# Kernel optimization log

Measured on AMD Instinct MI355X. Metric: run time of the kernel, lower is better.

The kernel has to match this reference:

```python
import jax, jax.numpy as jnp
import numpy as np

B, D3, L, H, O, E, GH = 4096, 288, 32, 512, 96, 8, 128


def _init_linear(key, out_dim, in_dim):
    kw, kb = jax.random.split(key)
    bound = 1.0 / np.sqrt(in_dim)
    W = jax.random.uniform(kw, (out_dim, in_dim), jnp.float32, -bound, bound)
    b = jax.random.uniform(kb, (out_dim,), jnp.float32, -bound, bound)
    return W, b


def setup_inputs() -> dict:
    key = jax.random.key(0)
    ks = jax.random.split(key, 12)
    x = jax.random.normal(ks[0], (B, D3), jnp.float32)
    z = jax.random.normal(ks[1], (B, L), jnp.float32)
    # per-expert weights, stacked on leading expert axis [E, out, in]
    def expert_stack(k, out_dim, in_dim):
        Ws, bs = [], []
        for i in range(E):
            Wi, bi = _init_linear(jax.random.fold_in(k, i), out_dim, in_dim)
            Ws.append(Wi); bs.append(bi)
        return jnp.stack(Ws), jnp.stack(bs)
    W0, b0 = expert_stack(ks[2], H, D3 + L)
    W1, b1 = expert_stack(ks[3], H, H + L)
    W2, b2 = expert_stack(ks[4], H, H + L)
    W3, b3 = expert_stack(ks[5], O, H)
    gW1, gb1 = _init_linear(ks[6], GH, D3 + L)
    gW2, gb2 = _init_linear(ks[7], GH, GH)
    gW3, gb3 = _init_linear(ks[8], E, GH)
    return {"x": x, "z": z, "W0": W0, "b0": b0, "W1": W1, "b1": b1,
            "W2": W2, "b2": b2, "W3": W3, "b3": b3,
            "gW1": gW1, "gb1": gb1, "gW2": gW2, "gb2": gb2,
            "gW3": gW3, "gb3": gb3}


def _gating(x, z, gW1, gb1, gW2, gb2, gW3, gb3):
    h = jnp.concatenate([x, z], axis=1)
    h = jax.nn.elu(h @ gW1.T + gb1)
    h = jax.nn.elu(h @ gW2.T + gb2)
    return jax.nn.softmax(h @ gW3.T + gb3, axis=-1)  # [B, E]


def _blended_linear(g, W, b, h):
    # Original: materializes sum_e g[b,e] * W_e -> [B,out,in], then bmm.
    # Mathematically identical linear form: sum_e g[b,e] * (W_e h_b + b_e).
    return jnp.einsum('be,eoi,bi->bo', g, W, h) + g @ b


def reference(x, z, W0, b0, W1, b1, W2, b2, W3, b3,
              gW1, gb1, gW2, gb2, gW3, gb3):
    g = _gating(x, z, gW1, gb1, gW2, gb2, gW3, gb3)  # [B, E]
    # dropout p=0.0 (eval) -> identity
    h = jax.nn.elu(_blended_linear(g, W0, b0, jnp.concatenate([x, z], axis=1)))
    h = jax.nn.elu(_blended_linear(g, W1, b1, jnp.concatenate([h, z], axis=1)))
    h = jax.nn.elu(_blended_linear(g, W2, b2, jnp.concatenate([h, z], axis=1)))
    out = _blended_linear(g, W3, b3, h)
    return out  # [B, O]
```

## Files before the change

kernel.cpp:

```cpp
#include <hip/hip_runtime.h>
#include <hip/hip_fp16.h>

typedef _Float16 half8 __attribute__((ext_vector_type(8)));
typedef _Float16 half4 __attribute__((ext_vector_type(4)));
typedef float floatx4 __attribute__((ext_vector_type(4)));

__device__ __forceinline__ void async_ld16(const void* g, void* l) {
    __builtin_amdgcn_global_load_lds(
        (const __attribute__((address_space(1))) char*)g,
        (__attribute__((address_space(3))) char*)l, 16, 0, 0);
}

__device__ __forceinline__ float elu_f(float v) {
    return v > 0.f ? v : expm1f(v);
}

__global__ void prep_kernel(const float* __restrict__ x, const float* __restrict__ z,
                            const float* __restrict__ W0, const float* __restrict__ W1,
                            const float* __restrict__ W2, const float* __restrict__ W3,
                            const float* __restrict__ gW1, const float* __restrict__ gW2,
                            const float* __restrict__ gW3,
                            _Float16* __restrict__ X0,
                            _Float16* __restrict__ h0, _Float16* __restrict__ h1,
                            _Float16* __restrict__ h2,
                            _Float16* __restrict__ Wc0, _Float16* __restrict__ Wc1,
                            _Float16* __restrict__ Wc2, _Float16* __restrict__ Wc3,
                            _Float16* __restrict__ gW1c, _Float16* __restrict__ gW2c,
                            _Float16* __restrict__ gW3c)
{
    const int N_X4  = 4096 * 288 / 4;
    const int N_Z4  = 4096 * 32 / 4;
    const int N_W04 = 8 * 512 * 320 / 4;
    const int N_W124 = 8 * 512 * 544 / 4;
    const int N_W34 = 8 * 96 * 512 / 4;
    const int N_G14 = 128 * 320 / 4, N_G24 = 128 * 128 / 4, N_G34 = 8 * 128 / 4;
    const int TOTAL4 = N_X4 + N_Z4 + 3 * N_Z4 + N_W04 + 2 * N_W124 + N_W34
                     + N_G14 + N_G24 + N_G34;

    auto cvt = [](const float* src, int j4) -> half4 {
        float4 f = ((const float4*)src)[j4];
        half4 h; h.x = (_Float16)f.x; h.y = (_Float16)f.y;
        h.z = (_Float16)f.z; h.w = (_Float16)f.w; return h;
    };

    for (int i = blockIdx.x * blockDim.x + threadIdx.x; i < TOTAL4;
         i += gridDim.x * blockDim.x) {
        int j = i;
        if (j < N_X4) {
            int b = j / 72, k4 = j - b * 72;
            *(half4*)(X0 + b * 320 + k4 * 4) = cvt(x, j);
            continue;
        }
        j -= N_X4;
        if (j < N_Z4) {
            int b = j / 8, k4 = j - b * 8;
            *(half4*)(X0 + b * 320 + 288 + k4 * 4) = cvt(z, j);
            continue;
        }
        j -= N_Z4;
        if (j < 3 * N_Z4) {
            int buf = j / N_Z4; int r = j - buf * N_Z4;
            int b = r / 8, k4 = r - b * 8;
            _Float16* h = (buf == 0) ? h0 : ((buf == 1) ? h1 : h2);
            *(half4*)(h + b * 544 + 512 + k4 * 4) = cvt(z, r);
            continue;
        }
        j -= 3 * N_Z4;
        if (j < N_W04)  { *(half4*)(Wc0 + j * 4) = cvt(W0, j); continue; } j -= N_W04;
        if (j < N_W124) { *(half4*)(Wc1 + j * 4) = cvt(W1, j); continue; } j -= N_W124;
        if (j < N_W124) { *(half4*)(Wc2 + j * 4) = cvt(W2, j); continue; } j -= N_W124;
        if (j < N_W34)  { *(half4*)(Wc3 + j * 4) = cvt(W3, j); continue; } j -= N_W34;
        if (j < N_G14)  { *(half4*)(gW1c + j * 4) = cvt(gW1, j); continue; } j -= N_G14;
        if (j < N_G24)  { *(half4*)(gW2c + j * 4) = cvt(gW2, j); continue; } j -= N_G24;
        *(half4*)(gW3c + j * 4) = cvt(gW3, j);
    }
}

__launch_bounds__(256)
__global__ void gating_fused(const _Float16* __restrict__ X0,
                             const _Float16* __restrict__ gW1c,
                             const _Float16* __restrict__ gW2c,
                             const _Float16* __restrict__ gW3c,
                             const float* __restrict__ gb1,
                             const float* __restrict__ gb2,
                             const float* __restrict__ gb3,
                             float* __restrict__ g)
{
    __shared__ _Float16 sA[128 * 32];
    __shared__ _Float16 sB[128 * 32];
    __shared__ _Float16 h1t[128 * 136];
    __shared__ _Float16 sW3[8 * 128];

    const int tid = threadIdx.x;
    const int l = tid & 63;
    const int w = tid >> 6;
    const int wm = w >> 1, wn = w & 1;
    const int m0 = blockIdx.x * 128;

    for (int t = tid; t < 8 * 128; t += 256) sW3[t] = gW3c[t];

    const int sub = l >> 2;
    const int kc  = (l & 3) * 8;
    const int row0 = w * 16 + sub;
    const _Float16* gA0 = X0 + (size_t)(m0 + row0) * 320 + kc;
    const _Float16* gA1 = gA0 + (size_t)64 * 320;
    const _Float16* gB0 = gW1c + (size_t)row0 * 320 + kc;
    const _Float16* gB1 = gW1c + (size_t)(row0 + 64) * 320 + kc;
    _Float16* sA0 = sA + w * 512;
    _Float16* sA1 = sA + 2048 + w * 512;
    _Float16* sB0 = sB + w * 512;
    _Float16* sB1 = sB + 2048 + w * 512;

    const int mi = l & 15, quad = l >> 4;
    const _Float16* rA = sA + (wm * 64 + mi) * 32 + quad * 8;
    const _Float16* rB = sB + (wn * 64 + mi) * 32 + quad * 8;

    floatx4 acc[4][4] = {};

    for (int k0 = 0; k0 < 320; k0 += 32) {
        __syncthreads();
        async_ld16(gA0 + k0, sA0);
        async_ld16(gA1 + k0, sA1);
        async_ld16(gB0 + k0, sB0);
        async_ld16(gB1 + k0, sB1);
        __syncthreads();
        half8 af[4], bf[4];
#pragma unroll
        for (int i = 0; i < 4; i++) af[i] = *(const half8*)(rA + i * 16 * 32);
#pragma unroll
        for (int j = 0; j < 4; j++) bf[j] = *(const half8*)(rB + j * 16 * 32);
#pragma unroll
        for (int i = 0; i < 4; i++)
#pragma unroll
            for (int j = 0; j < 4; j++)
                acc[i][j] = __builtin_amdgcn_mfma_f32_16x16x32_f16(af[i], bf[j], acc[i][j], 0, 0, 0);
    }
    __syncthreads();
#pragma unroll
    for (int i = 0; i < 4; i++)
#pragma unroll
        for (int j = 0; j < 4; j++) {
            int n = wn * 64 + j * 16 + mi;
            float bn = gb1[n];
#pragma unroll
            for (int r = 0; r < 4; r++) {
                int mrel = wm * 64 + i * 16 + quad * 4 + r;
                h1t[mrel * 136 + n] = (_Float16)elu_f(acc[i][j][r] + bn);
            }
        }

    floatx4 acc2[4][4] = {};
    const _Float16* gB20 = gW2c + (size_t)row0 * 128 + kc;
    const _Float16* gB21 = gW2c + (size_t)(row0 + 64) * 128 + kc;
    const _Float16* rA2b = h1t + (wm * 64 + mi) * 136 + quad * 8;
    for (int ks = 0; ks < 4; ks++) {
        __syncthreads();
        async_ld16(gB20 + ks * 32, sB0);
        async_ld16(gB21 + ks * 32, sB1);
        __syncthreads();
        half8 af[4], bf[4];
#pragma unroll
        for (int i = 0; i < 4; i++) af[i] = *(const half8*)(rA2b + i * 16 * 136 + ks * 32);
#pragma unroll
        for (int j = 0; j < 4; j++) bf[j] = *(const half8*)(rB + j * 16 * 32);
#pragma unroll
        for (int i = 0; i < 4; i++)
#pragma unroll
            for (int j = 0; j < 4; j++)
                acc2[i][j] = __builtin_amdgcn_mfma_f32_16x16x32_f16(af[i], bf[j], acc2[i][j], 0, 0, 0);
    }
    __syncthreads();
#pragma unroll
    for (int i = 0; i < 4; i++)
#pragma unroll
        for (int j = 0; j < 4; j++) {
            int n = wn * 64 + j * 16 + mi;
            float bn = gb2[n];
#pragma unroll
            for (int r = 0; r < 4; r++) {
                int mrel = wm * 64 + i * 16 + quad * 4 + r;
                h1t[mrel * 136 + n] = (_Float16)elu_f(acc2[i][j][r] + bn);
            }
        }
    __syncthreads();

    const int e = l >> 3, kk = l & 7;
    for (int rr = 0; rr < 32; rr++) {
        int row = w * 32 + rr;
        const _Float16* hr = h1t + row * 136 + kk * 16;
        const _Float16* wr = sW3 + e * 128 + kk * 16;
        half8 hv0 = *(const half8*)hr;
        half8 hv1 = *(const half8*)(hr + 8);
        half8 wv0 = *(const half8*)wr;
        half8 wv1 = *(const half8*)(wr + 8);
        float s = 0.f;
#pragma unroll
        for (int t = 0; t < 8; t++)
            s += (float)hv0[t] * (float)wv0[t] + (float)hv1[t] * (float)wv1[t];
        s += __shfl_xor(s, 1);
        s += __shfl_xor(s, 2);
        s += __shfl_xor(s, 4);
        float logit = s + gb3[e];
        float mx = logit;
        mx = fmaxf(mx, __shfl_xor(mx, 8));
        mx = fmaxf(mx, __shfl_xor(mx, 16));
        mx = fmaxf(mx, __shfl_xor(mx, 32));
        float ve = __expf(logit - mx);
        float ssum = ve;
        ssum += __shfl_xor(ssum, 1);
        ssum += __shfl_xor(ssum, 2);
        ssum += __shfl_xor(ssum, 4);
        ssum += __shfl_xor(ssum, 8);
        ssum += __shfl_xor(ssum, 16);
        ssum += __shfl_xor(ssum, 32);
        float gv = ve / (ssum * 0.125f);
        if (kk == 0) g[(size_t)(m0 + row) * 8 + e] = gv;
    }
}

template <bool ELU_ACT, typename OUT_T>
__launch_bounds__(256, 4)
__global__ void gemm_blend(const _Float16* __restrict__ A, int lda,
                           const _Float16* __restrict__ W, int ldw,
                           int Hdim, int K,
                           const float* __restrict__ g,
                           const float* __restrict__ bias,
                           OUT_T* __restrict__ out, int ldo)
{
    __shared__ __align__(16) char smem_raw[16384];
    _Float16* sA = (_Float16*)smem_raw;
    _Float16* sB = (_Float16*)(smem_raw + 8192);
    float* sredf = (float*)smem_raw;
    __shared__ float sg[128][9];
    __shared__ float sbias[8][16];

    const int tid = threadIdx.x;
    const int l = tid & 63;
    const int w = tid >> 6;
    const int wm = w >> 1, wn = w & 1;
    const int o0 = blockIdx.x * 16;
    const int m0 = blockIdx.y * 128;

    for (int t = tid; t < 128 * 8; t += 256)
        sg[t >> 3][t & 7] = g[(size_t)(m0 + (t >> 3)) * 8 + (t & 7)];
    for (int t = tid; t < 128; t += 256)
        sbias[t >> 4][t & 15] = bias[(t >> 4) * Hdim + o0 + (t & 15)];

    const int sub = l >> 2;
    const int kc  = (l & 3) * 8;
    const int row0 = w * 16 + sub;
    const _Float16* gA0 = A + (size_t)(m0 + row0) * lda + kc;
    const _Float16* gA1 = gA0 + (size_t)64 * lda;
    const int c0 = row0, c1 = row0 + 64;
    const _Float16* gB0 = W + (size_t)((c0 >> 4) * Hdim + o0 + (c0 & 15)) * ldw + kc;
    const _Float16* gB1 = W + (size_t)((c1 >> 4) * Hdim + o0 + (c1 & 15)) * ldw + kc;
    _Float16* sA0 = sA + w * 512;
    _Float16* sA1 = sA + 2048 + w * 512;
    _Float16* sB0 = sB + w * 512;
    _Float16* sB1 = sB + 2048 + w * 512;

    const int mi = l & 15, quad = l >> 4;
    const _Float16* rA = sA + (wm * 64 + mi) * 32 + quad * 8;
    const _Float16* rB = sB + (wn * 64 + mi) * 32 + quad * 8;

    floatx4 acc[4][4] = {};

    for (int k0 = 0; k0 < K; k0 += 32) {
        __syncthreads();
        async_ld16(gA0 + k0, sA0);
        async_ld16(gA1 + k0, sA1);
        async_ld16(gB0 + k0, sB0);
        async_ld16(gB1 + k0, sB1);
        __syncthreads();
        half8 af[4], bf[4];
#pragma unroll
        for (int i = 0; i < 4; i++) af[i] = *(const half8*)(rA + i * 16 * 32);
#pragma unroll
        for (int j = 0; j < 4; j++) bf[j] = *(const half8*)(rB + j * 16 * 32);
#pragma unroll
        for (int i = 0; i < 4; i++)
#pragma unroll
            for (int j = 0; j < 4; j++)
                acc[i][j] = __builtin_amdgcn_mfma_f32_16x16x32_f16(af[i], bf[j], acc[i][j], 0, 0, 0);
    }

    float p[4][4];
#pragma unroll
    for (int i = 0; i < 4; i++)
#pragma unroll
        for (int r = 0; r < 4; r++) {
            int mloc = wm * 64 + i * 16 + quad * 4 + r;
            float s = 0.f;
#pragma unroll
            for (int j = 0; j < 4; j++) {
                int e = wn * 4 + j;
                s += sg[mloc][e] * (acc[i][j][r] + sbias[e][mi]);
            }
            p[i][r] = s;
        }

    __syncthreads();
    if (wn == 0) {
#pragma unroll
        for (int i = 0; i < 4; i++)
#pragma unroll
            for (int r = 0; r < 4; r++)
                sredf[(wm * 64 + i * 16 + quad * 4 + r) * 17 + mi] = p[i][r];
    }
    __syncthreads();
    if (wn == 1) {
#pragma unroll
        for (int i = 0; i < 4; i++)
#pragma unroll
            for (int r = 0; r < 4; r++) {
                int mrel = i * 16 + quad * 4 + r;
                float v = p[i][r] + sredf[(wm * 64 + mrel) * 17 + mi];
                if (ELU_ACT) v = elu_f(v);
                out[(size_t)(m0 + wm * 64 + mrel) * ldo + o0 + mi] = (OUT_T)v;
            }
    }
}

extern "C" void kernel_launch(void* const* d_in, const int* in_sizes, int n_in,
                              void* d_out, int out_size, void* d_ws, size_t ws_size,
                              hipStream_t stream)
{
    (void)in_sizes; (void)n_in; (void)out_size; (void)ws_size;
    const float* x   = (const float*)d_in[0];
    const float* z   = (const float*)d_in[1];
    const float* W0  = (const float*)d_in[2];
    const float* b0  = (const float*)d_in[3];
    const float* W1  = (const float*)d_in[4];
    const float* b1  = (const float*)d_in[5];
    const float* W2  = (const float*)d_in[6];
    const float* b2  = (const float*)d_in[7];
    const float* W3  = (const float*)d_in[8];
    const float* b3  = (const float*)d_in[9];
    const float* gW1 = (const float*)d_in[10];
    const float* gb1 = (const float*)d_in[11];
    const float* gW2 = (const float*)d_in[12];
    const float* gb2 = (const float*)d_in[13];
    const float* gW3 = (const float*)d_in[14];
    const float* gb3 = (const float*)d_in[15];

    char* p = (char*)d_ws;
    auto alloc = [&](size_t n) { char* r = p; p += (n + 255) & ~(size_t)255; return r; };
    _Float16* X0   = (_Float16*)alloc((size_t)4096 * 320 * 2);
    _Float16* h0   = (_Float16*)alloc((size_t)4096 * 544 * 2);
    _Float16* h1   = (_Float16*)alloc((size_t)4096 * 544 * 2);
    _Float16* h2   = (_Float16*)alloc((size_t)4096 * 544 * 2);
    _Float16* Wc0  = (_Float16*)alloc((size_t)8 * 512 * 320 * 2);
    _Float16* Wc1  = (_Float16*)alloc((size_t)8 * 512 * 544 * 2);
    _Float16* Wc2  = (_Float16*)alloc((size_t)8 * 512 * 544 * 2);
    _Float16* Wc3  = (_Float16*)alloc((size_t)8 * 96 * 512 * 2);
    _Float16* gW1c = (_Float16*)alloc((size_t)128 * 320 * 2);
    _Float16* gW2c = (_Float16*)alloc((size_t)128 * 128 * 2);
    _Float16* gW3c = (_Float16*)alloc((size_t)8 * 128 * 2);
    float*    g    = (float*)alloc((size_t)4096 * 8 * 4);

    prep_kernel<<<2048, 256, 0, stream>>>(x, z, W0, W1, W2, W3, gW1, gW2, gW3,
                                          X0, h0, h1, h2, Wc0, Wc1, Wc2, Wc3,
                                          gW1c, gW2c, gW3c);

    gating_fused<<<32, 256, 0, stream>>>(X0, gW1c, gW2c, gW3c, gb1, gb2, gb3, g);

    gemm_blend<true, _Float16><<<dim3(32, 32), 256, 0, stream>>>(X0, 320, Wc0, 320, 512, 320, g, b0, h0, 544);
    gemm_blend<true, _Float16><<<dim3(32, 32), 256, 0, stream>>>(h0, 544, Wc1, 544, 512, 544, g, b1, h1, 544);
    gemm_blend<true, _Float16><<<dim3(32, 32), 256, 0, stream>>>(h1, 544, Wc2, 544, 512, 544, g, b2, h2, 544);
    gemm_blend<false, float><<<dim3(6, 32), 256, 0, stream>>>(h2, 544, Wc3, 512, 96, 512, g, b3, (float*)d_out, 96);
}
```

Measured before the change: 234.4 us.

## Fuse blend layers into persistent kernel with grid barriers; overlap weight conversion with gating

The four per-layer blend GEMM launches become one persistent kernel that steps through the layers, with a software grid barrier between them. The gating stage keeps its 32 blocks, and the remaining blocks of that launch convert the expert weights to fp16 at the same time, so the conversion no longer runs serially before gating. This removes launch gaps and the serial weight-conversion pass. In exchange it depends on all 1024 blocks being co-resident for the spin barrier, which risks deadlock or atomic spin overhead.

```diff
diff --git a/kernel.cpp b/kernel.cpp
--- a/kernel.cpp
+++ b/kernel.cpp
@@ -15,46 +15,55 @@
     return v > 0.f ? v : expm1f(v);
 }
 
-__global__ void prep_kernel(const float* __restrict__ x, const float* __restrict__ z,
-                            const float* __restrict__ W0, const float* __restrict__ W1,
-                            const float* __restrict__ W2, const float* __restrict__ W3,
-                            const float* __restrict__ gW1, const float* __restrict__ gW2,
-                            const float* __restrict__ gW3,
-                            _Float16* __restrict__ X0,
-                            _Float16* __restrict__ h0, _Float16* __restrict__ h1,
-                            _Float16* __restrict__ h2,
-                            _Float16* __restrict__ Wc0, _Float16* __restrict__ Wc1,
-                            _Float16* __restrict__ Wc2, _Float16* __restrict__ Wc3,
-                            _Float16* __restrict__ gW1c, _Float16* __restrict__ gW2c,
-                            _Float16* __restrict__ gW3c)
+__device__ __forceinline__ void grid_barrier(unsigned int* bar, unsigned int target) {
+    __syncthreads();
+    if (threadIdx.x == 0) {
+        __threadfence();
+        atomicAdd(bar, 1u);
+        while (__hip_atomic_load(bar, __ATOMIC_ACQUIRE, __HIP_MEMORY_SCOPE_AGENT) < target)
+            __builtin_amdgcn_s_sleep(1);
+        __threadfence();
+    }
+    __syncthreads();
+}
+
+__device__ __forceinline__ half4 cvt4(const float* src, int j4) {
+    float4 f = ((const float4*)src)[j4];
+    half4 h; h.x = (_Float16)f.x; h.y = (_Float16)f.y;
+    h.z = (_Float16)f.z; h.w = (_Float16)f.w; return h;
+}
+
+__global__ void prep_light(const float* __restrict__ x, const float* __restrict__ z,
+                           const float* __restrict__ gW1, const float* __restrict__ gW2,
+                           const float* __restrict__ gW3,
+                           _Float16* __restrict__ X0,
+                           _Float16* __restrict__ h0, _Float16* __restrict__ h1,
+                           _Float16* __restrict__ h2,
+                           _Float16* __restrict__ gW1c, _Float16* __restrict__ gW2c,
+                           _Float16* __restrict__ gW3c,
+                           unsigned int* __restrict__ bars)
 {
+    if (blockIdx.x == 0 && threadIdx.x < 8) bars[threadIdx.x] = 0u;
+
     const int N_X4  = 4096 * 288 / 4;
     const int N_Z4  = 4096 * 32 / 4;
-    const int N_W04 = 8 * 512 * 320 / 4;
-    const int N_W124 = 8 * 512 * 544 / 4;
-    const int N_W34 = 8 * 96 * 512 / 4;
-    const int N_G14 = 128 * 320 / 4, N_G24 = 128 * 128 / 4, N_G34 = 8 * 128 / 4;
-    const int TOTAL4 = N_X4 + N_Z4 + 3 * N_Z4 + N_W04 + 2 * N_W124 + N_W34
-                     + N_G14 + N_G24 + N_G34;
-
-    auto cvt = [](const float* src, int j4) -> half4 {
-        float4 f = ((const float4*)src)[j4];
-        half4 h; h.x = (_Float16)f.x; h.y = (_Float16)f.y;
-        h.z = (_Float16)f.z; h.w = (_Float16)f.w; return h;
-    };
+    const int N_G14 = 128 * 320 / 4;
+    const int N_G24 = 128 * 128 / 4;
+    const int N_G34 = 8 * 128 / 4;
+    const int TOTAL4 = N_X4 + 4 * N_Z4 + N_G14 + N_G24 + N_G34;
 
     for (int i = blockIdx.x * blockDim.x + threadIdx.x; i < TOTAL4;
          i += gridDim.x * blockDim.x) {
         int j = i;
         if (j < N_X4) {
             int b = j / 72, k4 = j - b * 72;
-            *(half4*)(X0 + b * 320 + k4 * 4) = cvt(x, j);
+            *(half4*)(X0 + b * 320 + k4 * 4) = cvt4(x, j);
             continue;
         }
         j -= N_X4;
         if (j < N_Z4) {
             int b = j / 8, k4 = j - b * 8;
-            *(half4*)(X0 + b * 320 + 288 + k4 * 4) = cvt(z, j);
+            *(half4*)(X0 + b * 320 + 288 + k4 * 4) = cvt4(z, j);
             continue;
         }
         j -= N_Z4;
@@ -62,29 +71,29 @@
             int buf = j / N_Z4; int r = j - buf * N_Z4;
             int b = r / 8, k4 = r - b * 8;
             _Float16* h = (buf == 0) ? h0 : ((buf == 1) ? h1 : h2);
-            *(half4*)(h + b * 544 + 512 + k4 * 4) = cvt(z, r);
+            *(half4*)(h + b * 544 + 512 + k4 * 4) = cvt4(z, r);
             continue;
         }
         j -= 3 * N_Z4;
-        if (j < N_W04)  { *(half4*)(Wc0 + j * 4) = cvt(W0, j); continue; } j -= N_W04;
-        if (j < N_W124) { *(half4*)(Wc1 + j * 4) = cvt(W1, j); continue; } j -= N_W124;
-        if (j < N_W124) { *(half4*)(Wc2 + j * 4) = cvt(W2, j); continue; } j -= N_W124;
-        if (j < N_W34)  { *(half4*)(Wc3 + j * 4) = cvt(W3, j); continue; } j -= N_W34;
-        if (j < N_G14)  { *(half4*)(gW1c + j * 4) = cvt(gW1, j); continue; } j -= N_G14;
-        if (j < N_G24)  { *(half4*)(gW2c + j * 4) = cvt(gW2, j); continue; } j -= N_G24;
-        *(half4*)(gW3c + j * 4) = cvt(gW3, j);
+        if (j < N_G14) { *(half4*)(gW1c + j * 4) = cvt4(gW1, j); continue; } j -= N_G14;
+        if (j < N_G24) { *(half4*)(gW2c + j * 4) = cvt4(gW2, j); continue; } j -= N_G24;
+        *(half4*)(gW3c + j * 4) = cvt4(gW3, j);
     }
 }
 
 __launch_bounds__(256)
-__global__ void gating_fused(const _Float16* __restrict__ X0,
-                             const _Float16* __restrict__ gW1c,
-                             const _Float16* __restrict__ gW2c,
-                             const _Float16* __restrict__ gW3c,
-                             const float* __restrict__ gb1,
-                             const float* __restrict__ gb2,
-                             const float* __restrict__ gb3,
-                             float* __restrict__ g)
+__global__ void gating_and_wconv(const _Float16* __restrict__ X0,
+                                 const _Float16* __restrict__ gW1c,
+                                 const _Float16* __restrict__ gW2c,
+                                 const _Float16* __restrict__ gW3c,
+                                 const float* __restrict__ gb1,
+                                 const float* __restrict__ gb2,
+                                 const float* __restrict__ gb3,
+                                 float* __restrict__ g,
+                                 const float* __restrict__ W0, const float* __restrict__ W1,
+                                 const float* __restrict__ W2, const float* __restrict__ W3,
+                                 _Float16* __restrict__ Wc0, _Float16* __restrict__ Wc1,
+                                 _Float16* __restrict__ Wc2, _Float16* __restrict__ Wc3)
 {
     __shared__ _Float16 sA[128 * 32];
     __shared__ _Float16 sB[128 * 32];
@@ -92,6 +101,24 @@
     __shared__ _Float16 sW3[8 * 128];
 
     const int tid = threadIdx.x;
+
+    if (blockIdx.x >= 32) {
+        const int N_W04  = 8 * 512 * 320 / 4;
+        const int N_W124 = 8 * 512 * 544 / 4;
+        const int N_W34  = 8 * 96 * 512 / 4;
+        const int TOTAL4 = N_W04 + 2 * N_W124 + N_W34;
+        const int nb = gridDim.x - 32;
+        for (int i = (blockIdx.x - 32) * blockDim.x + tid; i < TOTAL4;
+             i += nb * blockDim.x) {
+            int j = i;
+            if (j < N_W04)  { *(half4*)(Wc0 + j * 4) = cvt4(W0, j); continue; } j -= N_W04;
+            if (j < N_W124) { *(half4*)(Wc1 + j * 4) = cvt4(W1, j); continue; } j -= N_W124;
+            if (j < N_W124) { *(half4*)(Wc2 + j * 4) = cvt4(W2, j); continue; } j -= N_W124;
+            *(half4*)(Wc3 + j * 4) = cvt4(W3, j);
+        }
+        return;
+    }
+
     const int l = tid & 63;
     const int w = tid >> 6;
     const int wm = w >> 1, wn = w & 1;
@@ -219,30 +246,23 @@
 }
 
 template <bool ELU_ACT, typename OUT_T>
-__launch_bounds__(256, 4)
-__global__ void gemm_blend(const _Float16* __restrict__ A, int lda,
-                           const _Float16* __restrict__ W, int ldw,
-                           int Hdim, int K,
-                           const float* __restrict__ g,
-                           const float* __restrict__ bias,
-                           OUT_T* __restrict__ out, int ldo)
+__device__ __forceinline__ void blend_tile(
+    const _Float16* __restrict__ A, int lda,
+    const _Float16* __restrict__ W, int ldw, int Hdim, int K,
+    const float* __restrict__ bias,
+    OUT_T* __restrict__ out, int ldo,
+    int m0, int o0,
+    char* smem_raw, float (*sg)[9], float (*sbias)[16])
 {
-    __shared__ __align__(16) char smem_raw[16384];
     _Float16* sA = (_Float16*)smem_raw;
     _Float16* sB = (_Float16*)(smem_raw + 8192);
     float* sredf = (float*)smem_raw;
-    __shared__ float sg[128][9];
-    __shared__ float sbias[8][16];
 
     const int tid = threadIdx.x;
     const int l = tid & 63;
     const int w = tid >> 6;
     const int wm = w >> 1, wn = w & 1;
-    const int o0 = blockIdx.x * 16;
-    const int m0 = blockIdx.y * 128;
-
-    for (int t = tid; t < 128 * 8; t += 256)
-        sg[t >> 3][t & 7] = g[(size_t)(m0 + (t >> 3)) * 8 + (t & 7)];
+
     for (int t = tid; t < 128; t += 256)
         sbias[t >> 4][t & 15] = bias[(t >> 4) * Hdim + o0 + (t & 15)];
 
@@ -318,6 +338,51 @@
                 if (ELU_ACT) v = elu_f(v);
                 out[(size_t)(m0 + wm * 64 + mrel) * ldo + o0 + mi] = (OUT_T)v;
             }
+    }
+}
+
+__launch_bounds__(256, 4)
+__global__ void mega_blend(const _Float16* __restrict__ X0,
+                           _Float16* __restrict__ h0, _Float16* __restrict__ h1,
+                           _Float16* __restrict__ h2,
+                           const _Float16* __restrict__ Wc0, const _Float16* __restrict__ Wc1,
+                           const _Float16* __restrict__ Wc2, const _Float16* __restrict__ Wc3,
+                           const float* __restrict__ g,
+                           const float* __restrict__ b0, const float* __restrict__ b1,
+                           const float* __restrict__ b2, const float* __restrict__ b3,
+                           float* __restrict__ out,
+                           unsigned int* __restrict__ bars)
+{
+    __shared__ __align__(16) char smem_raw[16384];
+    __shared__ float sg[128][9];
+    __shared__ float sbias[8][16];
+
+    const int tid = threadIdx.x;
+    const int id = blockIdx.x;
+    const int bx = id & 31, by = id >> 5;
+    const int m0 = by * 128, o0 = bx * 16;
+    const unsigned int nb = gridDim.x;
+
+    for (int t = tid; t < 128 * 8; t += 256)
+        sg[t >> 3][t & 7] = g[(size_t)(m0 + (t >> 3)) * 8 + (t & 7)];
+
+    blend_tile<true, _Float16>(X0, 320, Wc0, 320, 512, 320, b0, h0, 544, m0, o0,
+                               smem_raw, sg, sbias);
+    grid_barrier(&bars[0], nb);
+    blend_tile<true, _Float16>(h0, 544, Wc1, 544, 512, 544, b1, h1, 544, m0, o0,
+                               smem_raw, sg, sbias);
+    grid_barrier(&bars[1], nb);
+    blend_tile<true, _Float16>(h1, 544, Wc2, 544, 512, 544, b2, h2, 544, m0, o0,
+                               smem_raw, sg, sbias);
+    grid_barrier(&bars[2], nb);
+
+    if (id < 192) {
+        const int by4 = id / 6, bx4 = id - by4 * 6;
+        const int m04 = by4 * 128, o04 = bx4 * 16;
+        for (int t = tid; t < 128 * 8; t += 256)
+            sg[t >> 3][t & 7] = g[(size_t)(m04 + (t >> 3)) * 8 + (t & 7)];
+        blend_tile<false, float>(h2, 544, Wc3, 512, 96, 512, b3, out, 96, m04, o04,
+                                 smem_raw, sg, sbias);
     }
 }
 
@@ -357,15 +422,14 @@
     _Float16* gW2c = (_Float16*)alloc((size_t)128 * 128 * 2);
     _Float16* gW3c = (_Float16*)alloc((size_t)8 * 128 * 2);
     float*    g    = (float*)alloc((size_t)4096 * 8 * 4);
-
-    prep_kernel<<<2048, 256, 0, stream>>>(x, z, W0, W1, W2, W3, gW1, gW2, gW3,
-                                          X0, h0, h1, h2, Wc0, Wc1, Wc2, Wc3,
-                                          gW1c, gW2c, gW3c);
-
-    gating_fused<<<32, 256, 0, stream>>>(X0, gW1c, gW2c, gW3c, gb1, gb2, gb3, g);
-
-    gemm_blend<true, _Float16><<<dim3(32, 32), 256, 0, stream>>>(X0, 320, Wc0, 320, 512, 320, g, b0, h0, 544);
-    gemm_blend<true, _Float16><<<dim3(32, 32), 256, 0, stream>>>(h0, 544, Wc1, 544, 512, 544, g, b1, h1, 544);
-    gemm_blend<true, _Float16><<<dim3(32, 32), 256, 0, stream>>>(h1, 544, Wc2, 544, 512, 544, g, b2, h2, 544);
-    gemm_blend<false, float><<<dim3(6, 32), 256, 0, stream>>>(h2, 544, Wc3, 512, 96, 512, g, b3, (float*)d_out, 96);
-}
+    unsigned int* bars = (unsigned int*)alloc(8 * 4);
+
+    prep_light<<<512, 256, 0, stream>>>(x, z, gW1, gW2, gW3, X0, h0, h1, h2,
+                                        gW1c, gW2c, gW3c, bars);
+
+    gating_and_wconv<<<1024, 256, 0, stream>>>(X0, gW1c, gW2c, gW3c, gb1, gb2, gb3, g,
+                                               W0, W1, W2, W3, Wc0, Wc1, Wc2, Wc3);
+
+    mega_blend<<<1024, 256, 0, stream>>>(X0, h0, h1, h2, Wc0, Wc1, Wc2, Wc3, g,
+                                         b0, b1, b2, b3, (float*)d_out, bars);
+}
```

Result: slower. 638.4 us (+172.4%).

## Fuse prep into gating kernel and deepen GEMM K-tile with swizzled LDS

Applied to the files above, without the earlier changes.

Merges the fp32-to-fp16 conversion kernel with the gating kernel. The first 32 blocks compute gating straight from fp32 x/z/gW, and the remaining blocks convert the weights and activations. The blend GEMM now uses a K-step of 64 with XOR-swizzled shared memory, and hidden and weight row strides are padded to 576 so K is a multiple of 64. Two warps load A and two load B. This cuts one launch, halves the barrier count per K and reduces LDS bank conflicts, at the cost of double the LDS per block and possible occupancy loss.

```diff
diff --git a/kernel.cpp b/kernel.cpp
--- a/kernel.cpp
+++ b/kernel.cpp
@@ -15,101 +15,104 @@
     return v > 0.f ? v : expm1f(v);
 }
 
-__global__ void prep_kernel(const float* __restrict__ x, const float* __restrict__ z,
-                            const float* __restrict__ W0, const float* __restrict__ W1,
-                            const float* __restrict__ W2, const float* __restrict__ W3,
-                            const float* __restrict__ gW1, const float* __restrict__ gW2,
-                            const float* __restrict__ gW3,
-                            _Float16* __restrict__ X0,
-                            _Float16* __restrict__ h0, _Float16* __restrict__ h1,
-                            _Float16* __restrict__ h2,
-                            _Float16* __restrict__ Wc0, _Float16* __restrict__ Wc1,
-                            _Float16* __restrict__ Wc2, _Float16* __restrict__ Wc3,
-                            _Float16* __restrict__ gW1c, _Float16* __restrict__ gW2c,
-                            _Float16* __restrict__ gW3c)
+__device__ __forceinline__ half4 cvt4(const float* src, int j4) {
+    float4 f = ((const float4*)src)[j4];
+    half4 h; h.x = (_Float16)f.x; h.y = (_Float16)f.y;
+    h.z = (_Float16)f.z; h.w = (_Float16)f.w; return h;
+}
+
+__device__ __forceinline__ half8 cvt8(const float* src) {
+    float4 f0 = ((const float4*)src)[0];
+    float4 f1 = ((const float4*)src)[1];
+    half8 h;
+    h[0] = (_Float16)f0.x; h[1] = (_Float16)f0.y; h[2] = (_Float16)f0.z; h[3] = (_Float16)f0.w;
+    h[4] = (_Float16)f1.x; h[5] = (_Float16)f1.y; h[6] = (_Float16)f1.z; h[7] = (_Float16)f1.w;
+    return h;
+}
+
+__launch_bounds__(256)
+__global__ void gating_and_wconv(const float* __restrict__ x, const float* __restrict__ z,
+                                 const float* __restrict__ gW1, const float* __restrict__ gW2,
+                                 const float* __restrict__ gW3,
+                                 const float* __restrict__ gb1, const float* __restrict__ gb2,
+                                 const float* __restrict__ gb3,
+                                 float* __restrict__ g,
+                                 const float* __restrict__ W0, const float* __restrict__ W1,
+                                 const float* __restrict__ W2, const float* __restrict__ W3,
+                                 _Float16* __restrict__ X0,
+                                 _Float16* __restrict__ h0, _Float16* __restrict__ h1,
+                                 _Float16* __restrict__ h2,
+                                 _Float16* __restrict__ Wc0, _Float16* __restrict__ Wc1,
+                                 _Float16* __restrict__ Wc2, _Float16* __restrict__ Wc3)
 {
-    const int N_X4  = 4096 * 288 / 4;
-    const int N_Z4  = 4096 * 32 / 4;
-    const int N_W04 = 8 * 512 * 320 / 4;
-    const int N_W124 = 8 * 512 * 544 / 4;
-    const int N_W34 = 8 * 96 * 512 / 4;
-    const int N_G14 = 128 * 320 / 4, N_G24 = 128 * 128 / 4, N_G34 = 8 * 128 / 4;
-    const int TOTAL4 = N_X4 + N_Z4 + 3 * N_Z4 + N_W04 + 2 * N_W124 + N_W34
-                     + N_G14 + N_G24 + N_G34;
-
-    auto cvt = [](const float* src, int j4) -> half4 {
-        float4 f = ((const float4*)src)[j4];
-        half4 h; h.x = (_Float16)f.x; h.y = (_Float16)f.y;
-        h.z = (_Float16)f.z; h.w = (_Float16)f.w; return h;
-    };
-
-    for (int i = blockIdx.x * blockDim.x + threadIdx.x; i < TOTAL4;
-         i += gridDim.x * blockDim.x) {
-        int j = i;
-        if (j < N_X4) {
-            int b = j / 72, k4 = j - b * 72;
-            *(half4*)(X0 + b * 320 + k4 * 4) = cvt(x, j);
-            continue;
-        }
-        j -= N_X4;
-        if (j < N_Z4) {
-            int b = j / 8, k4 = j - b * 8;
-            *(half4*)(X0 + b * 320 + 288 + k4 * 4) = cvt(z, j);
-            continue;
-        }
-        j -= N_Z4;
-        if (j < 3 * N_Z4) {
-            int buf = j / N_Z4; int r = j - buf * N_Z4;
-            int b = r / 8, k4 = r - b * 8;
+    const int tid = threadIdx.x;
+
+    if (blockIdx.x >= 32) {
+        const int S0 = 294912;
+        const int S1 = 32768;
+        const int S2 = 327680;
+        const int S3 = 589824;
+        const int S4 = 589824;
+        const int S5 = 98304;
+        const int S6 = 196608;
+        const int TOTAL = S0 + S1 + S2 + S3 + S4 + S5 + S6;
+        const int nb = gridDim.x - 32;
+        const half4 hz = {};
+        for (int i = (blockIdx.x - 32) * blockDim.x + tid; i < TOTAL;
+             i += nb * blockDim.x) {
+            int j = i;
+            if (j < S0) {
+                int r = j / 72, c = j - r * 72;
+                *(half4*)(X0 + r * 320 + c * 4) = cvt4(x, j);
+                continue;
+            }
+            j -= S0;
+            if (j < S1) {
+                int r = j / 8, c = j - r * 8;
+                *(half4*)(X0 + r * 320 + 288 + c * 4) = cvt4(z, j);
+                continue;
+            }
+            j -= S1;
+            if (j < S2) { *(half4*)(Wc0 + j * 4) = cvt4(W0, j); continue; }
+            j -= S2;
+            if (j < S3) {
+                int r = j / 144, c = j - r * 144;
+                *(half4*)(Wc1 + r * 576 + c * 4) = (c < 136) ? cvt4(W1, r * 136 + c) : hz;
+                continue;
+            }
+            j -= S3;
+            if (j < S4) {
+                int r = j / 144, c = j - r * 144;
+                *(half4*)(Wc2 + r * 576 + c * 4) = (c < 136) ? cvt4(W2, r * 136 + c) : hz;
+                continue;
+            }
+            j -= S4;
+            if (j < S5) { *(half4*)(Wc3 + j * 4) = cvt4(W3, j); continue; }
+            j -= S5;
+            int buf = j >> 16;
+            int r2 = j & 65535;
+            int row = r2 >> 4, c = r2 & 15;
             _Float16* h = (buf == 0) ? h0 : ((buf == 1) ? h1 : h2);
-            *(half4*)(h + b * 544 + 512 + k4 * 4) = cvt(z, r);
-            continue;
-        }
-        j -= 3 * N_Z4;
-        if (j < N_W04)  { *(half4*)(Wc0 + j * 4) = cvt(W0, j); continue; } j -= N_W04;
-        if (j < N_W124) { *(half4*)(Wc1 + j * 4) = cvt(W1, j); continue; } j -= N_W124;
-        if (j < N_W124) { *(half4*)(Wc2 + j * 4) = cvt(W2, j); continue; } j -= N_W124;
-        if (j < N_W34)  { *(half4*)(Wc3 + j * 4) = cvt(W3, j); continue; } j -= N_W34;
-        if (j < N_G14)  { *(half4*)(gW1c + j * 4) = cvt(gW1, j); continue; } j -= N_G14;
-        if (j < N_G24)  { *(half4*)(gW2c + j * 4) = cvt(gW2, j); continue; } j -= N_G24;
-        *(half4*)(gW3c + j * 4) = cvt(gW3, j);
-    }
-}
-
-__launch_bounds__(256)
-__global__ void gating_fused(const _Float16* __restrict__ X0,
-                             const _Float16* __restrict__ gW1c,
-                             const _Float16* __restrict__ gW2c,
-                             const _Float16* __restrict__ gW3c,
-                             const float* __restrict__ gb1,
-                             const float* __restrict__ gb2,
-                             const float* __restrict__ gb3,
-                             float* __restrict__ g)
-{
+            *(half4*)(h + row * 576 + 512 + c * 4) = (c < 8) ? cvt4(z, row * 8 + c) : hz;
+        }
+        return;
+    }
+
     __shared__ _Float16 sA[128 * 32];
     __shared__ _Float16 sB[128 * 32];
     __shared__ _Float16 h1t[128 * 136];
     __shared__ _Float16 sW3[8 * 128];
 
-    const int tid = threadIdx.x;
     const int l = tid & 63;
     const int w = tid >> 6;
     const int wm = w >> 1, wn = w & 1;
     const int m0 = blockIdx.x * 128;
 
-    for (int t = tid; t < 8 * 128; t += 256) sW3[t] = gW3c[t];
+    for (int t = tid; t < 8 * 128; t += 256) sW3[t] = (_Float16)gW3[t];
 
     const int sub = l >> 2;
     const int kc  = (l & 3) * 8;
     const int row0 = w * 16 + sub;
-    const _Float16* gA0 = X0 + (size_t)(m0 + row0) * 320 + kc;
-    const _Float16* gA1 = gA0 + (size_t)64 * 320;
-    const _Float16* gB0 = gW1c + (size_t)row0 * 320 + kc;
-    const _Float16* gB1 = gW1c + (size_t)(row0 + 64) * 320 + kc;
-    _Float16* sA0 = sA + w * 512;
-    _Float16* sA1 = sA + 2048 + w * 512;
-    _Float16* sB0 = sB + w * 512;
-    _Float16* sB1 = sB + 2048 + w * 512;
 
     const int mi = l & 15, quad = l >> 4;
     const _Float16* rA = sA + (wm * 64 + mi) * 32 + quad * 8;
@@ -118,11 +121,21 @@
     floatx4 acc[4][4] = {};
 
     for (int k0 = 0; k0 < 320; k0 += 32) {
-        __syncthreads();
-        async_ld16(gA0 + k0, sA0);
-        async_ld16(gA1 + k0, sA1);
-        async_ld16(gB0 + k0, sB0);
-        async_ld16(gB1 + k0, sB1);
+        half8 a0, a1, b0, b1;
+        if (k0 < 288) {
+            a0 = cvt8(x + (size_t)(m0 + row0) * 288 + k0 + kc);
+            a1 = cvt8(x + (size_t)(m0 + row0 + 64) * 288 + k0 + kc);
+        } else {
+            a0 = cvt8(z + (size_t)(m0 + row0) * 32 + kc);
+            a1 = cvt8(z + (size_t)(m0 + row0 + 64) * 32 + kc);
+        }
+        b0 = cvt8(gW1 + (size_t)row0 * 320 + k0 + kc);
+        b1 = cvt8(gW1 + (size_t)(row0 + 64) * 320 + k0 + kc);
+        __syncthreads();
+        *(half8*)(sA + row0 * 32 + kc) = a0;
+        *(half8*)(sA + (row0 + 64) * 32 + kc) = a1;
+        *(half8*)(sB + row0 * 32 + kc) = b0;
+        *(half8*)(sB + (row0 + 64) * 32 + kc) = b1;
         __syncthreads();
         half8 af[4], bf[4];
 #pragma unroll
@@ -150,13 +163,13 @@
         }
 
     floatx4 acc2[4][4] = {};
-    const _Float16* gB20 = gW2c + (size_t)row0 * 128 + kc;
-    const _Float16* gB21 = gW2c + (size_t)(row0 + 64) * 128 + kc;
     const _Float16* rA2b = h1t + (wm * 64 + mi) * 136 + quad * 8;
     for (int ks = 0; ks < 4; ks++) {
-        __syncthreads();
-        async_ld16(gB20 + ks * 32, sB0);
-        async_ld16(gB21 + ks * 32, sB1);
+        half8 b0 = cvt8(gW2 + (size_t)row0 * 128 + ks * 32 + kc);
+        half8 b1 = cvt8(gW2 + (size_t)(row0 + 64) * 128 + ks * 32 + kc);
+        __syncthreads();
+        *(half8*)(sB + row0 * 32 + kc) = b0;
+        *(half8*)(sB + (row0 + 64) * 32 + kc) = b1;
         __syncthreads();
         half8 af[4], bf[4];
 #pragma unroll
@@ -220,16 +233,16 @@
 
 template <bool ELU_ACT, typename OUT_T>
 __launch_bounds__(256, 4)
-__global__ void gemm_blend(const _Float16* __restrict__ A, int lda,
-                           const _Float16* __restrict__ W, int ldw,
-                           int Hdim, int K,
-                           const float* __restrict__ g,
-                           const float* __restrict__ bias,
-                           OUT_T* __restrict__ out, int ldo)
+__global__ void blend64(const _Float16* __restrict__ A, int lda,
+                        const _Float16* __restrict__ W, int ldw,
+                        int Hdim, int K,
+                        const float* __restrict__ g,
+                        const float* __restrict__ bias,
+                        OUT_T* __restrict__ out, int ldo)
 {
-    __shared__ __align__(16) char smem_raw[16384];
+    __shared__ __align__(16) char smem_raw[32768];
     _Float16* sA = (_Float16*)smem_raw;
-    _Float16* sB = (_Float16*)(smem_raw + 8192);
+    _Float16* sB = (_Float16*)(smem_raw + 16384);
     float* sredf = (float*)smem_raw;
     __shared__ float sg[128][9];
     __shared__ float sbias[8][16];
@@ -246,42 +259,65 @@
     for (int t = tid; t < 128; t += 256)
         sbias[t >> 4][t & 15] = bias[(t >> 4) * Hdim + o0 + (t & 15)];
 
-    const int sub = l >> 2;
-    const int kc  = (l & 3) * 8;
-    const int row0 = w * 16 + sub;
-    const _Float16* gA0 = A + (size_t)(m0 + row0) * lda + kc;
-    const _Float16* gA1 = gA0 + (size_t)64 * lda;
-    const int c0 = row0, c1 = row0 + 64;
-    const _Float16* gB0 = W + (size_t)((c0 >> 4) * Hdim + o0 + (c0 & 15)) * ldw + kc;
-    const _Float16* gB1 = W + (size_t)((c1 >> 4) * Hdim + o0 + (c1 & 15)) * ldw + kc;
-    _Float16* sA0 = sA + w * 512;
-    _Float16* sA1 = sA + 2048 + w * 512;
-    _Float16* sB0 = sB + w * 512;
-    _Float16* sB1 = sB + 2048 + w * 512;
+    const int lr = l >> 3;
+    const int lc = l & 7;
+    const int swz = lc ^ lr;
+
+    const _Float16* gAp = A + (size_t)(m0 + w * 64 + lr) * lda + swz * 8;
+    _Float16* lAp = sA + w * 4096;
+    const int wb = w - 2;
+    const int eb = wb * 4;
+    const _Float16* gBe = W + ((size_t)eb * Hdim + o0 + lr) * ldw + swz * 8;
+    const _Float16* gBo = gBe + (size_t)8 * ldw;
+    _Float16* lBp = sB + wb * 4096;
 
     const int mi = l & 15, quad = l >> 4;
-    const _Float16* rA = sA + (wm * 64 + mi) * 32 + quad * 8;
-    const _Float16* rB = sB + (wn * 64 + mi) * 32 + quad * 8;
+    const int cswz = mi & 7;
+    const int offh0 = ((quad ^ cswz) * 8);
+    const int offh1 = (((quad + 4) ^ cswz) * 8);
+    const _Float16* rAb = sA + (wm * 64 + mi) * 64;
+    const _Float16* rBb = sB + (wn * 64 + mi) * 64;
 
     floatx4 acc[4][4] = {};
 
-    for (int k0 = 0; k0 < K; k0 += 32) {
-        __syncthreads();
-        async_ld16(gA0 + k0, sA0);
-        async_ld16(gA1 + k0, sA1);
-        async_ld16(gB0 + k0, sB0);
-        async_ld16(gB1 + k0, sB1);
-        __syncthreads();
-        half8 af[4], bf[4];
-#pragma unroll
-        for (int i = 0; i < 4; i++) af[i] = *(const half8*)(rA + i * 16 * 32);
-#pragma unroll
-        for (int j = 0; j < 4; j++) bf[j] = *(const half8*)(rB + j * 16 * 32);
-#pragma unroll
-        for (int i = 0; i < 4; i++)
-#pragma unroll
-            for (int j = 0; j < 4; j++)
-                acc[i][j] = __builtin_amdgcn_mfma_f32_16x16x32_f16(af[i], bf[j], acc[i][j], 0, 0, 0);
+    for (int k0 = 0; k0 < K; k0 += 64) {
+        __syncthreads();
+        if (w < 2) {
+            const _Float16* gp = gAp + k0;
+            _Float16* lp = lAp;
+#pragma unroll
+            for (int c = 0; c < 8; c++) {
+                async_ld16(gp, lp);
+                gp += (size_t)8 * lda;
+                lp += 512;
+            }
+        } else {
+            const _Float16* ge = gBe + k0;
+            const _Float16* go = gBo + k0;
+            _Float16* lp = lBp;
+#pragma unroll
+            for (int c2 = 0; c2 < 4; c2++) {
+                async_ld16(ge, lp); lp += 512;
+                async_ld16(go, lp); lp += 512;
+                ge += (size_t)Hdim * ldw;
+                go += (size_t)Hdim * ldw;
+            }
+        }
+        __syncthreads();
+#pragma unroll
+        for (int h = 0; h < 2; h++) {
+            const int off = h ? offh1 : offh0;
+            half8 af[4], bf[4];
+#pragma unroll
+            for (int i = 0; i < 4; i++) af[i] = *(const half8*)(rAb + i * 1024 + off);
+#pragma unroll
+            for (int j = 0; j < 4; j++) bf[j] = *(const half8*)(rBb + j * 1024 + off);
+#pragma unroll
+            for (int i = 0; i < 4; i++)
+#pragma unroll
+                for (int j = 0; j < 4; j++)
+                    acc[i][j] = __builtin_amdgcn_mfma_f32_16x16x32_f16(af[i], bf[j], acc[i][j], 0, 0, 0);
+        }
     }
 
     float p[4][4];
@@ -346,26 +382,21 @@
     char* p = (char*)d_ws;
     auto alloc = [&](size_t n) { char* r = p; p += (n + 255) & ~(size_t)255; return r; };
     _Float16* X0   = (_Float16*)alloc((size_t)4096 * 320 * 2);
-    _Float16* h0   = (_Float16*)alloc((size_t)4096 * 544 * 2);
-    _Float16* h1   = (_Float16*)alloc((size_t)4096 * 544 * 2);
-    _Float16* h2   = (_Float16*)alloc((size_t)4096 * 544 * 2);
+    _Float16* h0   = (_Float16*)alloc((size_t)4096 * 576 * 2);
+    _Float16* h1   = (_Float16*)alloc((size_t)4096 * 576 * 2);
+    _Float16* h2   = (_Float16*)alloc((size_t)4096 * 576 * 2);
     _Float16* Wc0  = (_Float16*)alloc((size_t)8 * 512 * 320 * 2);
-    _Float16* Wc1  = (_Float16*)alloc((size_t)8 * 512 * 544 * 2);
-    _Float16* Wc2  = (_Float16*)alloc((size_t)8 * 512 * 544 * 2);
+    _Float16* Wc1  = (_Float16*)alloc((size_t)8 * 512 * 576 * 2);
+    _Float16* Wc2  = (_Float16*)alloc((size_t)8 * 512 * 576 * 2);
     _Float16* Wc3  = (_Float16*)alloc((size_t)8 * 96 * 512 * 2);
-    _Float16* gW1c = (_Float16*)alloc((size_t)128 * 320 * 2);
-    _Float16* gW2c = (_Float16*)alloc((size_t)128 * 128 * 2);
-    _Float16* gW3c = (_Float16*)alloc((size_t)8 * 128 * 2);
     float*    g    = (float*)alloc((size_t)4096 * 8 * 4);
 
-    prep_kernel<<<2048, 256, 0, stream>>>(x, z, W0, W1, W2, W3, gW1, gW2, gW3,
-                                          X0, h0, h1, h2, Wc0, Wc1, Wc2, Wc3,
-                                          gW1c, gW2c, gW3c);
-
-    gating_fused<<<32, 256, 0, stream>>>(X0, gW1c, gW2c, gW3c, gb1, gb2, gb3, g);
-
-    gemm_blend<true, _Float16><<<dim3(32, 32), 256, 0, stream>>>(X0, 320, Wc0, 320, 512, 320, g, b0, h0, 544);
-    gemm_blend<true, _Float16><<<dim3(32, 32), 256, 0, stream>>>(h0, 544, Wc1, 544, 512, 544, g, b1, h1, 544);
-    gemm_blend<true, _Float16><<<dim3(32, 32), 256, 0, stream>>>(h1, 544, Wc2, 544, 512, 544, g, b2, h2, 544);
-    gemm_blend<false, float><<<dim3(6, 32), 256, 0, stream>>>(h2, 544, Wc3, 512, 96, 512, g, b3, (float*)d_out, 96);
-}
+    gating_and_wconv<<<1024, 256, 0, stream>>>(x, z, gW1, gW2, gW3, gb1, gb2, gb3, g,
+                                               W0, W1, W2, W3, X0, h0, h1, h2,
+                                               Wc0, Wc1, Wc2, Wc3);
+
+    blend64<true, _Float16><<<dim3(32, 32), 256, 0, stream>>>(X0, 320, Wc0, 320, 512, 320, g, b0, h0, 576);
+    blend64<true, _Float16><<<dim3(32, 32), 256, 0, stream>>>(h0, 576, Wc1, 576, 512, 576, g, b1, h1, 576);
+    blend64<true, _Float16><<<dim3(32, 32), 256, 0, stream>>>(h1, 576, Wc2, 576, 512, 576, g, b2, h2, 576);
+    blend64<false, float><<<dim3(6, 32), 256, 0, stream>>>(h2, 576, Wc3, 512, 96, 512, g, b3, (float*)d_out, 96);
+}
```

New measurement: 224.3 us. -4.3%, faster.
